# Optimization experiments

Hardware: AMD Instinct MI355X
Metric: run time of the kernel (lower is better)

Reference implementation:

```python
import jax, jax.numpy as jnp
import numpy as np

N = 50000
E = 800000
D_IN = 128
D_H = 128
D_OUT = 57
NEG_SLOPE = 0.2


def setup_inputs() -> dict:
    key = jax.random.key(0)
    ks = jax.random.split(key, 12)
    s_in = 1.0 / np.sqrt(D_IN)
    s_h = 1.0 / np.sqrt(D_H)
    return {
        "x": jax.random.normal(ks[0], (N, D_IN), jnp.float32),
        "edge_index": jax.random.randint(ks[1], (2, E), 0, N, jnp.int64),
        "W1": jax.random.normal(ks[2], (D_IN, D_H), jnp.float32) * s_in,
        "a1_src": jax.random.normal(ks[3], (D_H,), jnp.float32) * s_h,
        "a1_dst": jax.random.normal(ks[4], (D_H,), jnp.float32) * s_h,
        "b1": jnp.zeros((D_H,), jnp.float32),
        "W2": jax.random.normal(ks[5], (D_H, D_H), jnp.float32) * s_h,
        "a2_src": jax.random.normal(ks[6], (D_H,), jnp.float32) * s_h,
        "a2_dst": jax.random.normal(ks[7], (D_H,), jnp.float32) * s_h,
        "b2": jnp.zeros((D_H,), jnp.float32),
        "fc_w": jax.random.normal(ks[8], (D_H, D_OUT), jnp.float32) * s_h,
        "fc_b": jnp.zeros((D_OUT,), jnp.float32),
    }


def _gat_layer(x, src, dst, n, W, a_src, a_dst, b):
    """Single-head PyG GATConv (concat=True, heads=1). src/dst include self-loops."""
    h = x @ W                                # [N, Dh]
    alpha_s = h @ a_src                      # [N]
    alpha_d = h @ a_dst                      # [N]
    e = alpha_s[src] + alpha_d[dst]          # [E+N] per-edge logit
    e = jnp.where(e > 0, e, NEG_SLOPE * e)   # leaky_relu
    # segment softmax over incoming edges of each destination node
    m = jax.ops.segment_max(e, dst, num_segments=n)
    m = jnp.where(jnp.isfinite(m), m, 0.0)
    ex = jnp.exp(e - m[dst])
    den = jax.ops.segment_sum(ex, dst, num_segments=n)
    w = ex / den[dst]                        # [E+N] attention weights
    out = jax.ops.segment_sum(w[:, None] * h[src], dst, num_segments=n)
    return out + b


def reference(x, edge_index, W1, a1_src, a1_dst, b1, W2, a2_src, a2_dst, b2, fc_w, fc_b):
    n = x.shape[0]
    loops = jnp.arange(n, dtype=edge_index.dtype)
    src = jnp.concatenate([edge_index[0], loops])
    dst = jnp.concatenate([edge_index[1], loops])
    h = jax.nn.relu(_gat_layer(x, src, dst, n, W1, a1_src, a1_dst, b1))
    # dropout p=0.5 is identity in eval mode
    h = _gat_layer(h, src, dst, n, W2, a2_src, a2_dst, b2)
    return h @ fc_w + fc_b
```

## Files before the change

kernel.cpp:

```cpp
#include <hip/hip_runtime.h>


#define NEG_SLOPE 0.2f

__global__ void probe_i64_kernel(const int* __restrict__ ei, int E, int* __restrict__ flag)
{
    int lane = threadIdx.x;
    int v = 0;
    int lim = (E < 256) ? E : 256;
    for (int t = lane; t < lim; t += 64) v |= ei[2 * t + 1];
    #pragma unroll
    for (int o = 32; o >= 1; o >>= 1) v |= __shfl_xor(v, o);
    if (lane == 0) flag[0] = (v == 0) ? 1 : 0;
}


__global__ __launch_bounds__(256) void count_deg_kernel(
    const int* __restrict__ ei, int E, int n,
    const int* __restrict__ flag, int* __restrict__ deg)
{
    int is64 = flag[0];
    int i = blockIdx.x * blockDim.x + threadIdx.x;
    if (i >= E + n) return;
    int d;
    if (i < E) d = is64 ? ei[2 * (E + i)] : ei[E + i];
    else       d = i - E;
    atomicAdd(&deg[d], 1);
}

__global__ __launch_bounds__(1024) void scan1_kernel(
    const int* __restrict__ deg, int* __restrict__ rowptr,
    int* __restrict__ csum, int n)
{
    __shared__ int wsum[16];
    int b = blockIdx.x, tid = threadIdx.x;
    int lane = tid & 63, wv = tid >> 6;
    int i = b * 1024 + tid;
    int v = (i < n) ? deg[i] : 0;
    int s = v;
    #pragma unroll
    for (int off = 1; off < 64; off <<= 1) {
        int t = __shfl_up(s, off);
        if (lane >= off) s += t;
    }
    if (lane == 63) wsum[wv] = s;
    __syncthreads();
    if (wv == 0) {
        int ws = (lane < 16) ? wsum[lane] : 0;
        #pragma unroll
        for (int off = 1; off < 16; off <<= 1) {
            int t = __shfl_up(ws, off);
            if (lane >= off) ws += t;
        }
        if (lane < 16) wsum[lane] = ws;
    }
    __syncthreads();
    int woff = (wv == 0) ? 0 : wsum[wv - 1];
    int incl = woff + s;
    if (i < n) rowptr[i + 1] = incl;
    if (tid == 1023) csum[b] = incl;
    if (b == 0 && tid == 0) rowptr[0] = 0;
}

__global__ void scan2_kernel(int* __restrict__ csum, int nb)
{
    int lane = threadIdx.x;
    int v = (lane < nb) ? csum[lane] : 0;
    #pragma unroll
    for (int off = 1; off < 64; off <<= 1) {
        int t = __shfl_up(v, off);
        if (lane >= off) v += t;
    }
    if (lane < nb) csum[lane] = v;
}

__global__ __launch_bounds__(1024) void scan3_kernel(
    const int* __restrict__ csum, int* __restrict__ rowptr, int n)
{
    int b = blockIdx.x + 1;
    int i = b * 1024 + threadIdx.x;
    if (i < n) rowptr[i + 1] += csum[b - 1];
}

__global__ __launch_bounds__(256) void scatter_kernel(
    const int* __restrict__ ei, int E, int n,
    const int* __restrict__ flag,
    const int* __restrict__ rowptr, int* __restrict__ deg, int* __restrict__ col)
{
    int is64 = flag[0];
    int i = blockIdx.x * blockDim.x + threadIdx.x;
    if (i >= E + n) return;
    int s, d;
    if (i < E) {
        if (is64) { s = ei[2 * i]; d = ei[2 * (E + i)]; }
        else      { s = ei[i];     d = ei[E + i]; }
    } else {
        s = i - E; d = s;
    }
    int pos = atomicSub(&deg[d], 1) - 1;
    col[rowptr[d] + pos] = s;
}

__global__ __launch_bounds__(256) void gemm_h_kernel(
    const float* __restrict__ X, const float* __restrict__ W,
    const float* __restrict__ asv, const float* __restrict__ adv,
    float* __restrict__ H, float* __restrict__ As, float* __restrict__ Ad, int n)
{
    __shared__ float Wl[64 * 128];
    int tid = threadIdx.x;
    int cg = tid & 15, rg = tid >> 4;
    int row0 = blockIdx.x * 32;
    int r0 = row0 + rg * 2, r1 = r0 + 1;
    int rc0 = (r0 < n) ? r0 : (n - 1);
    int rc1 = (r1 < n) ? r1 : (n - 1);

    float acc[2][8];
    #pragma unroll
    for (int i = 0; i < 2; ++i)
        #pragma unroll
        for (int c = 0; c < 8; ++c) acc[i][c] = 0.f;

    const float4* Wl4 = (const float4*)Wl;

    #pragma unroll
    for (int p = 0; p < 2; ++p) {
        {
            const float4* W4 = (const float4*)(W + p * 64 * 128);
            float4* Wl4w = (float4*)Wl;
            #pragma unroll
            for (int t = 0; t < 8; ++t) Wl4w[tid + t * 256] = W4[tid + t * 256];
        }
        __syncthreads();

        const float* X0 = X + (size_t)rc0 * 128 + p * 64;
        const float* X1 = X + (size_t)rc1 * 128 + p * 64;
        for (int k = 0; k < 64; k += 4) {
            float4 xa = *(const float4*)(X0 + k);
            float4 xb = *(const float4*)(X1 + k);
            #pragma unroll
            for (int kk = 0; kk < 4; ++kk) {
                float4 wA = Wl4[(k + kk) * 32 + cg];
                float4 wB = Wl4[(k + kk) * 32 + 16 + cg];
                float x0s = (kk == 0) ? xa.x : (kk == 1) ? xa.y : (kk == 2) ? xa.z : xa.w;
                float x1s = (kk == 0) ? xb.x : (kk == 1) ? xb.y : (kk == 2) ? xb.z : xb.w;
                acc[0][0] += x0s * wA.x; acc[0][1] += x0s * wA.y;
                acc[0][2] += x0s * wA.z; acc[0][3] += x0s * wA.w;
                acc[0][4] += x0s * wB.x; acc[0][5] += x0s * wB.y;
                acc[0][6] += x0s * wB.z; acc[0][7] += x0s * wB.w;
                acc[1][0] += x1s * wA.x; acc[1][1] += x1s * wA.y;
                acc[1][2] += x1s * wA.z; acc[1][3] += x1s * wA.w;
                acc[1][4] += x1s * wB.x; acc[1][5] += x1s * wB.y;
                acc[1][6] += x1s * wB.z; acc[1][7] += x1s * wB.w;
            }
        }
        __syncthreads();
    }

    float4 asA = *(const float4*)(asv + cg * 4);
    float4 asB = *(const float4*)(asv + 64 + cg * 4);
    float4 adA = *(const float4*)(adv + cg * 4);
    float4 adB = *(const float4*)(adv + 64 + cg * 4);

    #pragma unroll
    for (int i = 0; i < 2; ++i) {
        int r = r0 + i;
        float ps = acc[i][0] * asA.x + acc[i][1] * asA.y + acc[i][2] * asA.z + acc[i][3] * asA.w
                 + acc[i][4] * asB.x + acc[i][5] * asB.y + acc[i][6] * asB.z + acc[i][7] * asB.w;
        float pd = acc[i][0] * adA.x + acc[i][1] * adA.y + acc[i][2] * adA.z + acc[i][3] * adA.w
                 + acc[i][4] * adB.x + acc[i][5] * adB.y + acc[i][6] * adB.z + acc[i][7] * adB.w;
        #pragma unroll
        for (int mask = 8; mask >= 1; mask >>= 1) {
            ps += __shfl_xor(ps, mask);
            pd += __shfl_xor(pd, mask);
        }
        if (r < n) {
            *(float4*)(H + (size_t)r * 128 + cg * 4)      = make_float4(acc[i][0], acc[i][1], acc[i][2], acc[i][3]);
            *(float4*)(H + (size_t)r * 128 + 64 + cg * 4) = make_float4(acc[i][4], acc[i][5], acc[i][6], acc[i][7]);
            if (cg == 0) { As[r] = ps; Ad[r] = pd; }
        }
    }
}


__global__ __launch_bounds__(256) void gat_agg_kernel(
    const float* __restrict__ H, const float* __restrict__ As, const float* __restrict__ Ad,
    const int* __restrict__ rowptr, const int* __restrict__ col,
    const float* __restrict__ bias, float* __restrict__ Out, int n, int relu)
{
    int wid = (blockIdx.x * blockDim.x + threadIdx.x) >> 6;
    int lane = threadIdx.x & 63;
    if (wid >= n) return;

    int beg = rowptr[wid], end = rowptr[wid + 1];
    int degn = end - beg;
    float adn = Ad[wid];

    int c0r = 0;
    if (lane < degn) c0r = col[beg + lane];

    float e0 = -1e30f;
    if (lane < degn) {
        float e = As[c0r] + adn;
        e0 = (e > 0.f) ? e : NEG_SLOPE * e;
    }
    float m = e0;
    for (int j = beg + lane + 64; j < end; j += 64) {
        float e = As[col[j]] + adn;
        e = (e > 0.f) ? e : NEG_SLOPE * e;
        m = fmaxf(m, e);
    }
    #pragma unroll
    for (int o = 32; o >= 1; o >>= 1) m = fmaxf(m, __shfl_xor(m, o));

    float ex0 = (lane < degn) ? __expf(e0 - m) : 0.f;
    float den = ex0;
    for (int j = beg + lane + 64; j < end; j += 64) {
        float e = As[col[j]] + adn;
        e = (e > 0.f) ? e : NEG_SLOPE * e;
        den += __expf(e - m);
    }
    #pragma unroll
    for (int o = 32; o >= 1; o >>= 1) den += __shfl_xor(den, o);
    float inv = 1.f / den;

    const float2* H2 = (const float2*)H;
    float accx = 0.f, accy = 0.f;
    int nfull = (degn < 64) ? degn : 64;
    int j = 0;
    for (; j + 4 <= nfull; j += 4) {
        int   s0 = __shfl(c0r, j),     s1 = __shfl(c0r, j + 1);
        int   s2 = __shfl(c0r, j + 2), s3 = __shfl(c0r, j + 3);
        float w0 = __shfl(ex0, j),     w1 = __shfl(ex0, j + 1);
        float w2 = __shfl(ex0, j + 2), w3 = __shfl(ex0, j + 3);
        float2 h0 = H2[(size_t)s0 * 64 + lane];
        float2 h1 = H2[(size_t)s1 * 64 + lane];
        float2 h2 = H2[(size_t)s2 * 64 + lane];
        float2 h3 = H2[(size_t)s3 * 64 + lane];
        accx += w0 * h0.x; accy += w0 * h0.y;
        accx += w1 * h1.x; accy += w1 * h1.y;
        accx += w2 * h2.x; accy += w2 * h2.y;
        accx += w3 * h3.x; accy += w3 * h3.y;
    }
    for (; j < nfull; ++j) {
        int s = __shfl(c0r, j);
        float w = __shfl(ex0, j);
        float2 hv = H2[(size_t)s * 64 + lane];
        accx += w * hv.x; accy += w * hv.y;
    }
    for (int jj = 64; jj < degn; ++jj) {
        int s = col[beg + jj];
        float e = As[s] + adn;
        e = (e > 0.f) ? e : NEG_SLOPE * e;
        float w = __expf(e - m);
        float2 hv = H2[(size_t)s * 64 + lane];
        accx += w * hv.x; accy += w * hv.y;
    }

    float2 b2 = ((const float2*)bias)[lane];
    float ox = accx * inv + b2.x;
    float oy = accy * inv + b2.y;
    if (relu) { ox = fmaxf(ox, 0.f); oy = fmaxf(oy, 0.f); }
    float2 o2; o2.x = ox; o2.y = oy;
    ((float2*)Out)[(size_t)wid * 64 + lane] = o2;
}

__global__ __launch_bounds__(256) void fc_kernel(
    const float* __restrict__ H, const float* __restrict__ Wf,
    const float* __restrict__ bf, float* __restrict__ Out, int n)
{
    __shared__ float Wl[128 * 64];
    int tid = threadIdx.x;
    for (int i = tid; i < 128 * 64; i += 256) {
        int k = i >> 6, c = i & 63;
        Wl[i] = (c < 57) ? Wf[k * 57 + c] : 0.f;
    }
    __syncthreads();

    int cg = tid & 15, rg = tid >> 4;
    int c0 = cg * 4;
    int row0 = blockIdx.x * 32;
    int r0 = row0 + rg * 2, r1 = r0 + 1;
    int rc0 = (r0 < n) ? r0 : (n - 1);
    int rc1 = (r1 < n) ? r1 : (n - 1);

    float acc[2][4];
    #pragma unroll
    for (int i = 0; i < 2; ++i)
        #pragma unroll
        for (int c = 0; c < 4; ++c) acc[i][c] = 0.f;

    const float* X0 = H + (size_t)rc0 * 128;
    const float* X1 = H + (size_t)rc1 * 128;
    const float4* Wl4 = (const float4*)Wl;

    for (int k = 0; k < 128; k += 4) {
        float4 xa = *(const float4*)(X0 + k);
        float4 xb = *(const float4*)(X1 + k);
        #pragma unroll
        for (int kk = 0; kk < 4; ++kk) {
            float4 wv = Wl4[(k + kk) * 16 + cg];
            float x0s = (kk == 0) ? xa.x : (kk == 1) ? xa.y : (kk == 2) ? xa.z : xa.w;
            float x1s = (kk == 0) ? xb.x : (kk == 1) ? xb.y : (kk == 2) ? xb.z : xb.w;
            acc[0][0] += x0s * wv.x; acc[0][1] += x0s * wv.y;
            acc[0][2] += x0s * wv.z; acc[0][3] += x0s * wv.w;
            acc[1][0] += x1s * wv.x; acc[1][1] += x1s * wv.y;
            acc[1][2] += x1s * wv.z; acc[1][3] += x1s * wv.w;
        }
    }

    #pragma unroll
    for (int i = 0; i < 2; ++i) {
        int r = r0 + i;
        if (r >= n) continue;
        #pragma unroll
        for (int cc = 0; cc < 4; ++cc) {
            int c = c0 + cc;
            if (c < 57) Out[(size_t)r * 57 + c] = acc[i][cc] + bf[c];
        }
    }
}


extern "C" void kernel_launch(void* const* d_in, const int* in_sizes, int n_in,
                              void* d_out, int out_size, void* d_ws, size_t ws_size,
                              hipStream_t stream)
{
    const float* x   = (const float*)d_in[0];
    const int*   ei  = (const int*)d_in[1];
    const float* W1  = (const float*)d_in[2];
    const float* a1s = (const float*)d_in[3];
    const float* a1d = (const float*)d_in[4];
    const float* b1  = (const float*)d_in[5];
    const float* W2  = (const float*)d_in[6];
    const float* a2s = (const float*)d_in[7];
    const float* a2d = (const float*)d_in[8];
    const float* b2  = (const float*)d_in[9];
    const float* fcw = (const float*)d_in[10];
    const float* fcb = (const float*)d_in[11];
    float* out = (float*)d_out;

    int n = in_sizes[0] / 128;
    int E = in_sizes[1] / 2;
    int tot = E + n;
    int nchunks = (n + 1023) / 1024;

    char* ws = (char*)d_ws;
    size_t off = 0;
    auto alloc = [&](size_t bytes) -> void* {
        void* p = ws + off;
        off += (bytes + 255) & ~(size_t)255;
        return p;
    };
    float* hA     = (float*)alloc((size_t)n * 128 * 4);
    float* hB     = (float*)alloc((size_t)n * 128 * 4);
    float* As     = (float*)alloc((size_t)n * 4);
    float* Ad     = (float*)alloc((size_t)n * 4);
    int*   rowptr = (int*)alloc((size_t)(n + 1) * 4);
    int*   deg    = (int*)alloc((size_t)n * 4);
    int*   col    = (int*)alloc((size_t)tot * 4);
    int*   flag   = (int*)alloc(256);
    int*   csum   = (int*)alloc((size_t)64 * 4);

    hipMemsetAsync(deg, 0, (size_t)n * 4, stream);

    probe_i64_kernel<<<1, 64, 0, stream>>>(ei, E, flag);

    int nb = (tot + 255) / 256;
    count_deg_kernel<<<nb, 256, 0, stream>>>(ei, E, n, flag, deg);
    scan1_kernel<<<nchunks, 1024, 0, stream>>>(deg, rowptr, csum, n);
    scan2_kernel<<<1, 64, 0, stream>>>(csum, nchunks);
    if (nchunks > 1)
        scan3_kernel<<<nchunks - 1, 1024, 0, stream>>>(csum, rowptr, n);
    scatter_kernel<<<nb, 256, 0, stream>>>(ei, E, n, flag, rowptr, deg, col);

    int gb = (n + 31) / 32;
    int ab = (n + 3) / 4;

    gemm_h_kernel<<<gb, 256, 0, stream>>>(x, W1, a1s, a1d, hA, As, Ad, n);
    gat_agg_kernel<<<ab, 256, 0, stream>>>(hA, As, Ad, rowptr, col, b1, hB, n, 1);
    gemm_h_kernel<<<gb, 256, 0, stream>>>(hB, W2, a2s, a2d, hA, As, Ad, n);
    gat_agg_kernel<<<ab, 256, 0, stream>>>(hA, As, Ad, rowptr, col, b2, hB, n, 0);
    fc_kernel<<<gb, 256, 0, stream>>>(hB, fcw, fcb, out, n);
}
```

Baseline: 384.8 us.

## Store node features in fp16, drop softmax max pass, handle self-loops analytically

The GEMM now writes the projected features as fp16, halving the bytes gathered per edge in the aggregation kernel, which still accumulates in fp32. The segment-max pass of the softmax is removed and exp is applied to the raw logits, which saves a pass over each neighbour list but can overflow if logits get large. Self-loops are no longer atomically counted. They are added as +1 in the scan and written into the last slot of each row. The degree and scatter kernels also process two edges per thread, and the gather loop is unrolled to 8.

```diff
diff --git a/kernel.cpp b/kernel.cpp
--- a/kernel.cpp
+++ b/kernel.cpp
@@ -1,7 +1,10 @@
 #include <hip/hip_runtime.h>
+#include <hip/hip_fp16.h>
 
 
 #define NEG_SLOPE 0.2f
+
+struct __align__(8) half4_t { __half2 a, b; };
 
 __global__ void probe_i64_kernel(const int* __restrict__ ei, int E, int* __restrict__ flag)
 {
@@ -14,18 +17,27 @@
     if (lane == 0) flag[0] = (v == 0) ? 1 : 0;
 }
 
-
 __global__ __launch_bounds__(256) void count_deg_kernel(
     const int* __restrict__ ei, int E, int n,
     const int* __restrict__ flag, int* __restrict__ deg)
 {
     int is64 = flag[0];
-    int i = blockIdx.x * blockDim.x + threadIdx.x;
-    if (i >= E + n) return;
-    int d;
-    if (i < E) d = is64 ? ei[2 * (E + i)] : ei[E + i];
-    else       d = i - E;
-    atomicAdd(&deg[d], 1);
+    int half = (E + 1) >> 1;
+    int i2 = blockIdx.x * blockDim.x + threadIdx.x;
+    if (i2 >= half) return;
+    int e0 = 2 * i2;
+    bool has1 = (e0 + 1) < E;
+    int d0, d1 = 0;
+    if (is64) {
+        const int2* p = (const int2*)ei;
+        d0 = p[E + e0].x;
+        if (has1) d1 = p[E + e0 + 1].x;
+    } else {
+        d0 = ei[E + e0];
+        if (has1) d1 = ei[E + e0 + 1];
+    }
+    atomicAdd(&deg[d0], 1);
+    if (has1) atomicAdd(&deg[d1], 1);
 }
 
 __global__ __launch_bounds__(1024) void scan1_kernel(
@@ -36,7 +48,7 @@
     int b = blockIdx.x, tid = threadIdx.x;
     int lane = tid & 63, wv = tid >> 6;
     int i = b * 1024 + tid;
-    int v = (i < n) ? deg[i] : 0;
+    int v = (i < n) ? (deg[i] + 1) : 0;
     int s = v;
     #pragma unroll
     for (int off = 1; off < 64; off <<= 1) {
@@ -88,23 +100,36 @@
     const int* __restrict__ rowptr, int* __restrict__ deg, int* __restrict__ col)
 {
     int is64 = flag[0];
-    int i = blockIdx.x * blockDim.x + threadIdx.x;
-    if (i >= E + n) return;
-    int s, d;
-    if (i < E) {
-        if (is64) { s = ei[2 * i]; d = ei[2 * (E + i)]; }
-        else      { s = ei[i];     d = ei[E + i]; }
+    int half = (E + 1) >> 1;
+    int i2 = blockIdx.x * blockDim.x + threadIdx.x;
+    if (i2 < half) {
+        int e0 = 2 * i2;
+        bool has1 = (e0 + 1) < E;
+        int s0, d0, s1 = 0, d1 = 0;
+        if (is64) {
+            const int2* p = (const int2*)ei;
+            s0 = p[e0].x;     d0 = p[E + e0].x;
+            if (has1) { s1 = p[e0 + 1].x; d1 = p[E + e0 + 1].x; }
+        } else {
+            s0 = ei[e0];      d0 = ei[E + e0];
+            if (has1) { s1 = ei[e0 + 1];  d1 = ei[E + e0 + 1]; }
+        }
+        int pos0 = atomicSub(&deg[d0], 1) - 1;
+        col[rowptr[d0] + pos0] = s0;
+        if (has1) {
+            int pos1 = atomicSub(&deg[d1], 1) - 1;
+            col[rowptr[d1] + pos1] = s1;
+        }
     } else {
-        s = i - E; d = s;
-    }
-    int pos = atomicSub(&deg[d], 1) - 1;
-    col[rowptr[d] + pos] = s;
+        int d = i2 - half;
+        if (d < n) col[rowptr[d + 1] - 1] = d;
+    }
 }
 
 __global__ __launch_bounds__(256) void gemm_h_kernel(
     const float* __restrict__ X, const float* __restrict__ W,
     const float* __restrict__ asv, const float* __restrict__ adv,
-    float* __restrict__ H, float* __restrict__ As, float* __restrict__ Ad, int n)
+    __half* __restrict__ H16, float* __restrict__ As, float* __restrict__ Ad, int n)
 {
     __shared__ float Wl[64 * 128];
     int tid = threadIdx.x;
@@ -174,16 +199,20 @@
             pd += __shfl_xor(pd, mask);
         }
         if (r < n) {
-            *(float4*)(H + (size_t)r * 128 + cg * 4)      = make_float4(acc[i][0], acc[i][1], acc[i][2], acc[i][3]);
-            *(float4*)(H + (size_t)r * 128 + 64 + cg * 4) = make_float4(acc[i][4], acc[i][5], acc[i][6], acc[i][7]);
+            half4_t hlo, hhi;
+            hlo.a = __floats2half2_rn(acc[i][0], acc[i][1]);
+            hlo.b = __floats2half2_rn(acc[i][2], acc[i][3]);
+            hhi.a = __floats2half2_rn(acc[i][4], acc[i][5]);
+            hhi.b = __floats2half2_rn(acc[i][6], acc[i][7]);
+            *(half4_t*)(H16 + (size_t)r * 128 + cg * 4)      = hlo;
+            *(half4_t*)(H16 + (size_t)r * 128 + 64 + cg * 4) = hhi;
             if (cg == 0) { As[r] = ps; Ad[r] = pd; }
         }
     }
 }
 
-
 __global__ __launch_bounds__(256) void gat_agg_kernel(
-    const float* __restrict__ H, const float* __restrict__ As, const float* __restrict__ Ad,
+    const __half* __restrict__ H16, const float* __restrict__ As, const float* __restrict__ Ad,
     const int* __restrict__ rowptr, const int* __restrict__ col,
     const float* __restrict__ bias, float* __restrict__ Out, int n, int relu)
 {
@@ -198,62 +227,51 @@
     int c0r = 0;
     if (lane < degn) c0r = col[beg + lane];
 
-    float e0 = -1e30f;
+    float ex0 = 0.f;
     if (lane < degn) {
         float e = As[c0r] + adn;
-        e0 = (e > 0.f) ? e : NEG_SLOPE * e;
-    }
-    float m = e0;
-    for (int j = beg + lane + 64; j < end; j += 64) {
-        float e = As[col[j]] + adn;
         e = (e > 0.f) ? e : NEG_SLOPE * e;
-        m = fmaxf(m, e);
-    }
-    #pragma unroll
-    for (int o = 32; o >= 1; o >>= 1) m = fmaxf(m, __shfl_xor(m, o));
-
-    float ex0 = (lane < degn) ? __expf(e0 - m) : 0.f;
+        ex0 = __expf(e);
+    }
     float den = ex0;
     for (int j = beg + lane + 64; j < end; j += 64) {
         float e = As[col[j]] + adn;
         e = (e > 0.f) ? e : NEG_SLOPE * e;
-        den += __expf(e - m);
+        den += __expf(e);
     }
     #pragma unroll
     for (int o = 32; o >= 1; o >>= 1) den += __shfl_xor(den, o);
     float inv = 1.f / den;
 
-    const float2* H2 = (const float2*)H;
+    const __half2* H2 = (const __half2*)H16;
     float accx = 0.f, accy = 0.f;
     int nfull = (degn < 64) ? degn : 64;
     int j = 0;
-    for (; j + 4 <= nfull; j += 4) {
-        int   s0 = __shfl(c0r, j),     s1 = __shfl(c0r, j + 1);
-        int   s2 = __shfl(c0r, j + 2), s3 = __shfl(c0r, j + 3);
-        float w0 = __shfl(ex0, j),     w1 = __shfl(ex0, j + 1);
-        float w2 = __shfl(ex0, j + 2), w3 = __shfl(ex0, j + 3);
-        float2 h0 = H2[(size_t)s0 * 64 + lane];
-        float2 h1 = H2[(size_t)s1 * 64 + lane];
-        float2 h2 = H2[(size_t)s2 * 64 + lane];
-        float2 h3 = H2[(size_t)s3 * 64 + lane];
-        accx += w0 * h0.x; accy += w0 * h0.y;
-        accx += w1 * h1.x; accy += w1 * h1.y;
-        accx += w2 * h2.x; accy += w2 * h2.y;
-        accx += w3 * h3.x; accy += w3 * h3.y;
+    for (; j + 8 <= nfull; j += 8) {
+        int ss[8]; float ww[8]; __half2 hh[8];
+        #pragma unroll
+        for (int u = 0; u < 8; ++u) { ss[u] = __shfl(c0r, j + u); ww[u] = __shfl(ex0, j + u); }
+        #pragma unroll
+        for (int u = 0; u < 8; ++u) { hh[u] = H2[(size_t)ss[u] * 64 + lane]; }
+        #pragma unroll
+        for (int u = 0; u < 8; ++u) {
+            float2 f = __half22float2(hh[u]);
+            accx += ww[u] * f.x; accy += ww[u] * f.y;
+        }
     }
     for (; j < nfull; ++j) {
         int s = __shfl(c0r, j);
         float w = __shfl(ex0, j);
-        float2 hv = H2[(size_t)s * 64 + lane];
-        accx += w * hv.x; accy += w * hv.y;
+        float2 f = __half22float2(H2[(size_t)s * 64 + lane]);
+        accx += w * f.x; accy += w * f.y;
     }
     for (int jj = 64; jj < degn; ++jj) {
         int s = col[beg + jj];
         float e = As[s] + adn;
         e = (e > 0.f) ? e : NEG_SLOPE * e;
-        float w = __expf(e - m);
-        float2 hv = H2[(size_t)s * 64 + lane];
-        accx += w * hv.x; accy += w * hv.y;
+        float w = __expf(e);
+        float2 f = __half22float2(H2[(size_t)s * 64 + lane]);
+        accx += w * f.x; accy += w * f.y;
     }
 
     float2 b2 = ((const float2*)bias)[lane];
@@ -343,6 +361,7 @@
     int E = in_sizes[1] / 2;
     int tot = E + n;
     int nchunks = (n + 1023) / 1024;
+    int half = (E + 1) >> 1;
 
     char* ws = (char*)d_ws;
     size_t off = 0;
@@ -351,8 +370,8 @@
         off += (bytes + 255) & ~(size_t)255;
         return p;
     };
-    float* hA     = (float*)alloc((size_t)n * 128 * 4);
-    float* hB     = (float*)alloc((size_t)n * 128 * 4);
+    __half* h16   = (__half*)alloc((size_t)n * 128 * 2);
+    float* hF     = (float*)alloc((size_t)n * 128 * 4);
     float* As     = (float*)alloc((size_t)n * 4);
     float* Ad     = (float*)alloc((size_t)n * 4);
     int*   rowptr = (int*)alloc((size_t)(n + 1) * 4);
@@ -365,20 +384,21 @@
 
     probe_i64_kernel<<<1, 64, 0, stream>>>(ei, E, flag);
 
-    int nb = (tot + 255) / 256;
-    count_deg_kernel<<<nb, 256, 0, stream>>>(ei, E, n, flag, deg);
+    int cb = (half + 255) / 256;
+    count_deg_kernel<<<cb, 256, 0, stream>>>(ei, E, n, flag, deg);
     scan1_kernel<<<nchunks, 1024, 0, stream>>>(deg, rowptr, csum, n);
     scan2_kernel<<<1, 64, 0, stream>>>(csum, nchunks);
     if (nchunks > 1)
         scan3_kernel<<<nchunks - 1, 1024, 0, stream>>>(csum, rowptr, n);
-    scatter_kernel<<<nb, 256, 0, stream>>>(ei, E, n, flag, rowptr, deg, col);
+    int sb = (half + n + 255) / 256;
+    scatter_kernel<<<sb, 256, 0, stream>>>(ei, E, n, flag, rowptr, deg, col);
 
     int gb = (n + 31) / 32;
     int ab = (n + 3) / 4;
 
-    gemm_h_kernel<<<gb, 256, 0, stream>>>(x, W1, a1s, a1d, hA, As, Ad, n);
-    gat_agg_kernel<<<ab, 256, 0, stream>>>(hA, As, Ad, rowptr, col, b1, hB, n, 1);
-    gemm_h_kernel<<<gb, 256, 0, stream>>>(hB, W2, a2s, a2d, hA, As, Ad, n);
-    gat_agg_kernel<<<ab, 256, 0, stream>>>(hA, As, Ad, rowptr, col, b2, hB, n, 0);
-    fc_kernel<<<gb, 256, 0, stream>>>(hB, fcw, fcb, out, n);
-}
+    gemm_h_kernel<<<gb, 256, 0, stream>>>(x, W1, a1s, a1d, h16, As, Ad, n);
+    gat_agg_kernel<<<ab, 256, 0, stream>>>(h16, As, Ad, rowptr, col, b1, hF, n, 1);
+    gemm_h_kernel<<<gb, 256, 0, stream>>>(hF, W2, a2s, a2d, h16, As, Ad, n);
+    gat_agg_kernel<<<ab, 256, 0, stream>>>(h16, As, Ad, rowptr, col, b2, hF, n, 0);
+    fc_kernel<<<gb, 256, 0, stream>>>(hF, fcw, fcb, out, n);
+}
```

Result: faster. 353.6 us (-8.1%).
